# Performance work log

Measured on AMD Instinct MI355X. Metric: run time of the kernel, lower is better.

## Reference

```python
import jax, jax.numpy as jnp
import numpy as np

N = 8192      # neurons per layer (and n_inputs)
L = 16        # hidden topological layers
DEG = 128     # avg in-degree
E = N * DEG   # edges per hidden layer
NOUT = 16     # output neurons
EOUT = N * NOUT  # edges into output layer


def _lrelu(v):
    return jnp.where(v >= 0, v, 0.01 * v)


def setup_inputs() -> dict:
    key = jax.random.key(0)
    ks = jax.random.split(key, 7)
    x = jax.random.normal(ks[0], (N,), dtype=jnp.float32)
    edge_src = jax.random.randint(ks[1], (L, E), 0, N, dtype=jnp.int32)
    edge_dst = jax.random.randint(ks[2], (L, E), 0, N, dtype=jnp.int32)
    # scale weights ~1/sqrt(degree) so 16 layers of accumulation stay finite
    edge_w = jax.random.normal(ks[3], (L, E), dtype=jnp.float32) / np.float32(np.sqrt(DEG))
    out_src = jax.random.randint(ks[4], (EOUT,), 0, N, dtype=jnp.int32)
    out_dst = jax.random.randint(ks[5], (EOUT,), 0, NOUT, dtype=jnp.int32)
    out_w = jax.random.normal(ks[6], (EOUT,), dtype=jnp.float32) / np.float32(np.sqrt(EOUT / NOUT))
    return {"x": x, "edge_w": edge_w, "out_w": out_w,
            "edge_src": edge_src, "edge_dst": edge_dst,
            "out_src": out_src, "out_dst": out_dst}


def reference(x, edge_w, out_w, edge_src, edge_dst, out_src, out_dst):
    n = x.shape[0]

    def step(vals, layer):
        src, dst, w = layer
        # per-node weighted accumulation: n.value += i.value * i.weight[n]
        new = jax.ops.segment_sum(vals[src] * w, dst, num_segments=n)
        return _lrelu(new), None  # leaky_relu on every non-INPUT node

    vals, _ = jax.lax.scan(step, x, (edge_src, edge_dst, edge_w))
    o = jax.ops.segment_sum(vals[out_src] * out_w, out_dst, num_segments=NOUT)
    o = _lrelu(o)
    return jax.nn.softmax(o, axis=0)
```

## Files before the change

### kernel.cpp

```cpp
#include <hip/hip_runtime.h>

#define NN    8192
#define NL    16
#define NE    (NN * 128)
#define NOUTC 16
#define EOUTC (NN * NOUTC)

#define NBLK  256
#define NTHR  512
#define EPB   (NE / NBLK)

__device__ __forceinline__ float lrelu(float v) { return v >= 0.f ? v : 0.01f * v; }

__global__ __launch_bounds__(NTHR) void scatter_kernel(
    const float* __restrict__ sv,
    const int*   __restrict__ es,
    const int*   __restrict__ ed,
    const float* __restrict__ ew,
    float*       __restrict__ partials)
{
    __shared__ float vals[NN];
    __shared__ float accs[NN];
    const int tid = threadIdx.x;
    const int b   = blockIdx.x;

    for (int i = tid * 4; i < NN; i += NTHR * 4) {
        *(float4*)(vals + i) = *(const float4*)(sv + i);
        *(float4*)(accs + i) = make_float4(0.f, 0.f, 0.f, 0.f);
    }
    __syncthreads();

    const int base = b * EPB;
    #pragma unroll
    for (int it = 0; it < EPB / (NTHR * 4); ++it) {
        const int e = base + it * NTHR * 4 + tid * 4;
        int4   s = *(const int4*)(es + e);
        int4   d = *(const int4*)(ed + e);
        float4 w = *(const float4*)(ew + e);
        atomicAdd(&accs[d.x], vals[s.x] * w.x);
        atomicAdd(&accs[d.y], vals[s.y] * w.y);
        atomicAdd(&accs[d.z], vals[s.z] * w.z);
        atomicAdd(&accs[d.w], vals[s.w] * w.w);
    }
    __syncthreads();

    float* prow = partials + (size_t)b * NN;
    for (int i = tid * 4; i < NN; i += NTHR * 4)
        *(float4*)(prow + i) = *(const float4*)(accs + i);
}

__global__ __launch_bounds__(256) void reduce_kernel(
    const float* __restrict__ partials,
    float*       __restrict__ accv)
{
    __shared__ float sred[8][32];
    const int b  = blockIdx.x;
    const int nl = threadIdx.x & 31;
    const int kg = threadIdx.x >> 5;
    const int n  = b * 32 + nl;

    float s = 0.f;
    #pragma unroll
    for (int k = 0; k < NBLK / 8; ++k)
        s += partials[(size_t)(kg + k * 8) * NN + n];
    sred[kg][nl] = s;
    __syncthreads();
    if (threadIdx.x < 32) {
        float t = 0.f;
        #pragma unroll
        for (int j = 0; j < 8; ++j) t += sred[j][threadIdx.x];
        accv[b * 32 + threadIdx.x] = lrelu(t);
    }
}

__global__ __launch_bounds__(NTHR) void out_scatter_kernel(
    const float* __restrict__ accv,
    const int*   __restrict__ out_src,
    const int*   __restrict__ out_dst,
    const float* __restrict__ out_w,
    float*       __restrict__ outs)
{
    __shared__ float bins[NOUTC];
    const int tid = threadIdx.x;
    if (tid < NOUTC) bins[tid] = 0.f;
    __syncthreads();
    const int g = blockIdx.x * NTHR + tid;
    atomicAdd(&bins[out_dst[g]], accv[out_src[g]] * out_w[g]);
    __syncthreads();
    if (tid < NOUTC) outs[(size_t)blockIdx.x * NOUTC + tid] = bins[tid];
}

__global__ __launch_bounds__(256) void final_kernel(
    const float* __restrict__ outs, float* __restrict__ out)
{
    __shared__ float red[16][17];
    const int tid = threadIdx.x;
    const int j = tid & 15, g = tid >> 4;
    float s = 0.f;
    #pragma unroll
    for (int r = 0; r < NBLK / 16; ++r)
        s += outs[(size_t)(g + r * 16) * NOUTC + j];
    red[g][j] = s;
    __syncthreads();
    if (tid < NOUTC) {
        float t = 0.f;
        #pragma unroll
        for (int g2 = 0; g2 < 16; ++g2) t += red[g2][tid];
        float v = lrelu(t);
        float m = v;
        #pragma unroll
        for (int off = 8; off >= 1; off >>= 1)
            m = fmaxf(m, __shfl_xor(m, off, 64));
        float e = __expf(v - m);
        float ssum = e;
        #pragma unroll
        for (int off = 8; off >= 1; off >>= 1)
            ssum += __shfl_xor(ssum, off, 64);
        out[tid] = e / ssum;
    }
}

extern "C" void kernel_launch(void* const* d_in, const int* in_sizes, int n_in,
                              void* d_out, int out_size, void* d_ws, size_t ws_size,
                              hipStream_t stream) {
    const float* x        = (const float*)d_in[0];
    const float* edge_w   = (const float*)d_in[1];
    const float* out_w    = (const float*)d_in[2];
    const int*   edge_src = (const int*)d_in[3];
    const int*   edge_dst = (const int*)d_in[4];
    const int*   out_src  = (const int*)d_in[5];
    const int*   out_dst  = (const int*)d_in[6];

    float* partials = (float*)d_ws;
    float* accv     = partials + (size_t)NBLK * NN;
    float* outs     = accv + NN;
    float* out      = (float*)d_out;

    for (int l = 0; l < NL; ++l) {
        const float* sv = (l == 0) ? x : accv;
        scatter_kernel<<<NBLK, NTHR, 0, stream>>>(
            sv,
            edge_src + (size_t)l * NE,
            edge_dst + (size_t)l * NE,
            edge_w   + (size_t)l * NE,
            partials);
        reduce_kernel<<<NBLK, 256, 0, stream>>>(partials, accv);
    }

    out_scatter_kernel<<<NBLK, NTHR, 0, stream>>>(accv, out_src, out_dst, out_w, outs);
    final_kernel<<<1, 256, 0, stream>>>(outs, out);
}
```

Before: 404.4 us.

## Fuse all layers into one cooperative kernel using global atomics

New measurement: 1.479 ms. 266% more time.

```diff
diff --git a/kernel.cpp b/kernel.cpp
--- a/kernel.cpp
+++ b/kernel.cpp
@@ -1,4 +1,7 @@
 #include <hip/hip_runtime.h>
+#include <hip/hip_cooperative_groups.h>
+
+namespace cg = cooperative_groups;
 
 #define NN    8192
 #define NL    16
@@ -7,116 +10,112 @@
 #define EOUTC (NN * NOUTC)
 
 #define NBLK  256
-#define NTHR  512
+#define NTHR  1024
 #define EPB   (NE / NBLK)
+#define OPB   (EOUTC / NBLK)
 
 __device__ __forceinline__ float lrelu(float v) { return v >= 0.f ? v : 0.01f * v; }
 
-__global__ __launch_bounds__(NTHR) void scatter_kernel(
-    const float* __restrict__ sv,
-    const int*   __restrict__ es,
-    const int*   __restrict__ ed,
-    const float* __restrict__ ew,
-    float*       __restrict__ partials)
+__global__ __launch_bounds__(NTHR) void mega_kernel(
+    const float* __restrict__ x,
+    const float* __restrict__ edge_w,
+    const float* __restrict__ out_w,
+    const int*   __restrict__ edge_src,
+    const int*   __restrict__ edge_dst,
+    const int*   __restrict__ out_src,
+    const int*   __restrict__ out_dst,
+    float*       __restrict__ raw,
+    float*       __restrict__ outs,
+    float*       __restrict__ out)
 {
+    cg::grid_group grid = cg::this_grid();
     __shared__ float vals[NN];
-    __shared__ float accs[NN];
+    __shared__ float bins[NOUTC];
+    __shared__ float red[NOUTC][NOUTC + 1];
+
     const int tid = threadIdx.x;
     const int b   = blockIdx.x;
 
-    for (int i = tid * 4; i < NN; i += NTHR * 4) {
-        *(float4*)(vals + i) = *(const float4*)(sv + i);
-        *(float4*)(accs + i) = make_float4(0.f, 0.f, 0.f, 0.f);
+    const size_t e0 = (size_t)b * EPB + (size_t)tid * 4;
+    int4   s4 = *(const int4*)(edge_src + e0);
+    int4   d4 = *(const int4*)(edge_dst + e0);
+    float4 w4 = *(const float4*)(edge_w + e0);
+
+    {
+        const int g = b * NTHR + tid;
+        if (g < NL * NN) raw[g] = 0.f;
+    }
+    for (int i = tid * 4; i < NN; i += NTHR * 4)
+        *(float4*)(vals + i) = *(const float4*)(x + i);
+
+    grid.sync();
+
+    for (int l = 0; l < NL; ++l) {
+        float* r = raw + (size_t)l * NN;
+
+        const float cx = vals[s4.x] * w4.x;
+        const float cy = vals[s4.y] * w4.y;
+        const float cz = vals[s4.z] * w4.z;
+        const float cw = vals[s4.w] * w4.w;
+        atomicAdd(r + d4.x, cx);
+        atomicAdd(r + d4.y, cy);
+        atomicAdd(r + d4.z, cz);
+        atomicAdd(r + d4.w, cw);
+
+        if (l + 1 < NL) {
+            const size_t e = (size_t)(l + 1) * NE + (size_t)b * EPB + (size_t)tid * 4;
+            s4 = *(const int4*)(edge_src + e);
+            d4 = *(const int4*)(edge_dst + e);
+            w4 = *(const float4*)(edge_w + e);
+        }
+
+        grid.sync();
+
+        for (int i = tid * 4; i < NN; i += NTHR * 4) {
+            float4 v = *(const float4*)(r + i);
+            v.x = lrelu(v.x); v.y = lrelu(v.y);
+            v.z = lrelu(v.z); v.w = lrelu(v.w);
+            *(float4*)(vals + i) = v;
+        }
+        __syncthreads();
+    }
+
+    if (tid < NOUTC) bins[tid] = 0.f;
+    __syncthreads();
+    if (tid < OPB) {
+        const int e = b * OPB + tid;
+        atomicAdd(&bins[out_dst[e]], vals[out_src[e]] * out_w[e]);
     }
     __syncthreads();
+    if (tid < NOUTC) outs[(size_t)b * NOUTC + tid] = bins[tid];
+    grid.sync();
 
-    const int base = b * EPB;
-    #pragma unroll
-    for (int it = 0; it < EPB / (NTHR * 4); ++it) {
-        const int e = base + it * NTHR * 4 + tid * 4;
-        int4   s = *(const int4*)(es + e);
-        int4   d = *(const int4*)(ed + e);
-        float4 w = *(const float4*)(ew + e);
-        atomicAdd(&accs[d.x], vals[s.x] * w.x);
-        atomicAdd(&accs[d.y], vals[s.y] * w.y);
-        atomicAdd(&accs[d.z], vals[s.z] * w.z);
-        atomicAdd(&accs[d.w], vals[s.w] * w.w);
-    }
-    __syncthreads();
-
-    float* prow = partials + (size_t)b * NN;
-    for (int i = tid * 4; i < NN; i += NTHR * 4)
-        *(float4*)(prow + i) = *(const float4*)(accs + i);
-}
-
-__global__ __launch_bounds__(256) void reduce_kernel(
-    const float* __restrict__ partials,
-    float*       __restrict__ accv)
-{
-    __shared__ float sred[8][32];
-    const int b  = blockIdx.x;
-    const int nl = threadIdx.x & 31;
-    const int kg = threadIdx.x >> 5;
-    const int n  = b * 32 + nl;
-
-    float s = 0.f;
-    #pragma unroll
-    for (int k = 0; k < NBLK / 8; ++k)
-        s += partials[(size_t)(kg + k * 8) * NN + n];
-    sred[kg][nl] = s;
-    __syncthreads();
-    if (threadIdx.x < 32) {
-        float t = 0.f;
-        #pragma unroll
-        for (int j = 0; j < 8; ++j) t += sred[j][threadIdx.x];
-        accv[b * 32 + threadIdx.x] = lrelu(t);
-    }
-}
-
-__global__ __launch_bounds__(NTHR) void out_scatter_kernel(
-    const float* __restrict__ accv,
-    const int*   __restrict__ out_src,
-    const int*   __restrict__ out_dst,
-    const float* __restrict__ out_w,
-    float*       __restrict__ outs)
-{
-    __shared__ float bins[NOUTC];
-    const int tid = threadIdx.x;
-    if (tid < NOUTC) bins[tid] = 0.f;
-    __syncthreads();
-    const int g = blockIdx.x * NTHR + tid;
-    atomicAdd(&bins[out_dst[g]], accv[out_src[g]] * out_w[g]);
-    __syncthreads();
-    if (tid < NOUTC) outs[(size_t)blockIdx.x * NOUTC + tid] = bins[tid];
-}
-
-__global__ __launch_bounds__(256) void final_kernel(
-    const float* __restrict__ outs, float* __restrict__ out)
-{
-    __shared__ float red[16][17];
-    const int tid = threadIdx.x;
-    const int j = tid & 15, g = tid >> 4;
-    float s = 0.f;
-    #pragma unroll
-    for (int r = 0; r < NBLK / 16; ++r)
-        s += outs[(size_t)(g + r * 16) * NOUTC + j];
-    red[g][j] = s;
-    __syncthreads();
-    if (tid < NOUTC) {
-        float t = 0.f;
-        #pragma unroll
-        for (int g2 = 0; g2 < 16; ++g2) t += red[g2][tid];
-        float v = lrelu(t);
-        float m = v;
-        #pragma unroll
-        for (int off = 8; off >= 1; off >>= 1)
-            m = fmaxf(m, __shfl_xor(m, off, 64));
-        float e = __expf(v - m);
-        float ssum = e;
-        #pragma unroll
-        for (int off = 8; off >= 1; off >>= 1)
-            ssum += __shfl_xor(ssum, off, 64);
-        out[tid] = e / ssum;
+    if (b == 0) {
+        if (tid < 256) {
+            const int j = tid & 15, g = tid >> 4;
+            float s = 0.f;
+            #pragma unroll
+            for (int r2 = 0; r2 < NBLK / 16; ++r2)
+                s += outs[(size_t)(g + r2 * 16) * NOUTC + j];
+            red[g][j] = s;
+        }
+        __syncthreads();
+        if (tid < NOUTC) {
+            float t = 0.f;
+            #pragma unroll
+            for (int g2 = 0; g2 < 16; ++g2) t += red[g2][tid];
+            float v = lrelu(t);
+            float m = v;
+            #pragma unroll
+            for (int off = 8; off >= 1; off >>= 1)
+                m = fmaxf(m, __shfl_xor(m, off, 64));
+            const float e = __expf(v - m);
+            float ss = e;
+            #pragma unroll
+            for (int off = 8; off >= 1; off >>= 1)
+                ss += __shfl_xor(ss, off, 64);
+            out[tid] = e / ss;
+        }
     }
 }
 
@@ -131,22 +130,12 @@
     const int*   out_src  = (const int*)d_in[5];
     const int*   out_dst  = (const int*)d_in[6];
 
-    float* partials = (float*)d_ws;
-    float* accv     = partials + (size_t)NBLK * NN;
-    float* outs     = accv + NN;
-    float* out      = (float*)d_out;
+    float* raw  = (float*)d_ws;
+    float* outs = raw + (size_t)NL * NN;
+    float* out  = (float*)d_out;
 
-    for (int l = 0; l < NL; ++l) {
-        const float* sv = (l == 0) ? x : accv;
-        scatter_kernel<<<NBLK, NTHR, 0, stream>>>(
-            sv,
-            edge_src + (size_t)l * NE,
-            edge_dst + (size_t)l * NE,
-            edge_w   + (size_t)l * NE,
-            partials);
-        reduce_kernel<<<NBLK, 256, 0, stream>>>(partials, accv);
-    }
-
-    out_scatter_kernel<<<NBLK, NTHR, 0, stream>>>(accv, out_src, out_dst, out_w, outs);
-    final_kernel<<<1, 256, 0, stream>>>(outs, out);
+    void* args[] = {&x, &edge_w, &out_w, &edge_src, &edge_dst,
+                    &out_src, &out_dst, &raw, &outs, &out};
+    hipLaunchCooperativeKernel((void*)mega_kernel, dim3(NBLK), dim3(NTHR),
+                               args, 0, stream);
 }
```
